# Optimization experiments

Hardware: AMD Instinct MI355X
Metric: run time of the kernel (lower is better)

The kernel has to match this reference:

```python
import jax, jax.numpy as jnp
import numpy as np

NHEADS = 8
HEAD_DIM = 64  # odim // nheads = 512 // 8


def setup_inputs() -> dict:
    key = jax.random.key(0)
    ks = jax.random.split(key, 5)
    B, S, D = 2, 4096, 512
    scale = 1.0 / np.sqrt(D)
    return {
        "m_feats": jax.random.normal(ks[0], (B, S, D), dtype=jnp.float32),
        "Wc": jax.random.normal(ks[1], (2 * D, D), dtype=jnp.float32) * scale,
        "bc": jax.random.normal(ks[2], (2 * D,), dtype=jnp.float32) * 0.01,
        "Wv": jax.random.normal(ks[3], (D, D), dtype=jnp.float32) * scale,
        "bv": jax.random.normal(ks[4], (D,), dtype=jnp.float32) * 0.01,
    }


def reference(m_feats, Wc, bc, Wv, bv):
    # eval mode: dropout(p=0.5) is identity
    B, S, D = m_feats.shape
    H, Dh = NHEADS, HEAD_DIM
    m_k = m_feats @ Wv.T + bv                    # [B,S,D]
    m_trans = m_feats @ Wc.T + bc                # [B,S,2D]
    m_q, m_v = m_trans[..., :D], m_trans[..., D:]
    # torch.split into contiguous per-head chunks == reshape to [B,S,H,Dh]
    k = m_k.reshape(B, S, H, Dh)
    q = m_q.reshape(B, S, H, Dh)
    v = m_v.reshape(B, S, H, Dh)
    # scores[b,h,i,j] = k_i . q_j / sqrt(Dh); softmax over j (the q axis)
    scores = jnp.einsum("bihd,bjhd->bhij", k, q) / np.sqrt(Dh).astype(np.float32)
    w = jax.nn.softmax(scores, axis=-1)          # [B,H,S,S]
    r = jnp.einsum("bhij,bjhd->bihd", w, v).reshape(B, S, D)
    return m_feats + r
```

## Files before the change

### kernel.cpp

```cpp
#include <hip/hip_runtime.h>

#define MTOT 8192

typedef __attribute__((ext_vector_type(8))) short bf16x8;
typedef __attribute__((ext_vector_type(4))) float f32x4;

#if __has_builtin(__builtin_amdgcn_exp2f)
#define EXP2F __builtin_amdgcn_exp2f
#else
#define EXP2F exp2f
#endif

#define SC 0.18033688011112042f
#define LDP 72
#define CTS 136

static __device__ __forceinline__ unsigned short tb(float f) {
  union { float f; unsigned int i; } x;
  x.f = f;
  return (unsigned short)(x.i >> 16);
}
static __device__ __forceinline__ unsigned int pkt(float a, float b) {
  union { float f; unsigned int i; } xa, xb;
  xa.f = a; xb.f = b;
  return (xa.i >> 16) | (xb.i & 0xFFFF0000u);
}
static __device__ __forceinline__ bf16x8 ld8f32_bf16(const float* __restrict__ p) {
  f32x4 lo = *(const f32x4*)p;
  f32x4 hi = *(const f32x4*)(p + 4);
  union { unsigned int u[4]; bf16x8 v; } r;
  r.u[0] = pkt(lo[0], lo[1]);
  r.u[1] = pkt(lo[2], lo[3]);
  r.u[2] = pkt(hi[0], hi[1]);
  r.u[3] = pkt(hi[2], hi[3]);
  return r.v;
}

__global__ __launch_bounds__(256) void gemm_qvk(
    const float* __restrict__ mf,
    const float* __restrict__ Wc,
    const float* __restrict__ bc,
    const float* __restrict__ Wv,
    const float* __restrict__ bv,
    unsigned short* __restrict__ ws,
    int nct)
{
  const int bid = blockIdx.x;
  const int tn = bid % nct, tm = bid / nct;
  const int w = threadIdx.x >> 6, lane = threadIdx.x & 63;
  const int n = lane & 15, q = lane >> 4;

  __shared__ alignas(16) unsigned short smem[2 * 128 * LDP];
  unsigned short* As = smem;
  unsigned short* Bs = smem + 128 * LDP;

  f32x4 acc[4][4] = {};
  const int rowA0 = tm * 128, colB0 = tn * 128;
  const int sr = threadIdx.x >> 4;
  const int sc = (threadIdx.x & 15) * 4;

  for (int kc = 0; kc < 512; kc += 64) {
    __syncthreads();
#pragma unroll
    for (int rr = 0; rr < 8; ++rr) {
      const int row = rr * 16 + sr;
      f32x4 av = *(const f32x4*)(mf + (size_t)(rowA0 + row) * 512 + kc + sc);
      uint2 ap; ap.x = pkt(av[0], av[1]); ap.y = pkt(av[2], av[3]);
      *(uint2*)(&As[row * LDP + sc]) = ap;
      const int c = colB0 + row;
      const float* bsrc = (c < 1024) ? (Wc + (size_t)c * 512)
                                     : (Wv + (size_t)(c - 1024) * 512);
      f32x4 bvx = *(const f32x4*)(bsrc + kc + sc);
      uint2 bp; bp.x = pkt(bvx[0], bvx[1]); bp.y = pkt(bvx[2], bvx[3]);
      *(uint2*)(&Bs[row * LDP + sc]) = bp;
    }
    __syncthreads();
#pragma unroll
    for (int ks = 0; ks < 2; ++ks) {
      bf16x8 a[4], b[4];
#pragma unroll
      for (int si = 0; si < 4; ++si)
        a[si] = *(const bf16x8*)(&As[((w >> 1) * 64 + si * 16 + n) * LDP + ks * 32 + q * 8]);
#pragma unroll
      for (int sj = 0; sj < 4; ++sj)
        b[sj] = *(const bf16x8*)(&Bs[((w & 1) * 64 + sj * 16 + n) * LDP + ks * 32 + q * 8]);
#pragma unroll
      for (int si = 0; si < 4; ++si)
#pragma unroll
        for (int sj = 0; sj < 4; ++sj)
          acc[si][sj] = __builtin_amdgcn_mfma_f32_16x16x32_bf16(a[si], b[sj], acc[si][sj], 0, 0, 0);
    }
  }

  __syncthreads();
  unsigned short* Ct = smem;
  const bool isV = (tn >= 4 && tn < 8);
  const int rl0 = (w >> 1) * 64, cl0 = (w & 1) * 64;

  if (!isV) {
    const bool isK = (tn >= 8);
#pragma unroll
    for (int sj = 0; sj < 4; ++sj) {
      const int c = colB0 + sj * 16 + n;
      const float bias = isK ? bv[c - 1024] : bc[c];
#pragma unroll
      for (int si = 0; si < 4; ++si)
#pragma unroll
        for (int r = 0; r < 4; ++r) {
          float v = acc[si][sj][r] + bias;
          if (isK) v *= SC;
          Ct[(rl0 + si * 16 + q * 4 + r) * CTS + cl0 + sj * 16 + n] = tb(v);
        }
    }
  } else {
#pragma unroll
    for (int sj = 0; sj < 4; ++sj) {
      const float bias = bc[colB0 + sj * 16 + n];
#pragma unroll
      for (int si = 0; si < 4; ++si) {
        uint2 pk;
        pk.x = pkt(acc[si][sj][0] + bias, acc[si][sj][1] + bias);
        pk.y = pkt(acc[si][sj][2] + bias, acc[si][sj][3] + bias);
        *(uint2*)(&Ct[(cl0 + sj * 16 + n) * CTS + rl0 + si * 16 + q * 4]) = pk;
      }
    }
  }
  __syncthreads();

  const int rk = threadIdx.x & 7, rr2 = threadIdx.x >> 3;
#pragma unroll
  for (int rp = 0; rp < 4; ++rp) {
    const int row = rp * 32 + rr2;
#pragma unroll
    for (int ch = 0; ch < 2; ++ch) {
      const int col = ch * 64 + rk * 8;
      bf16x8 v = *(const bf16x8*)(&Ct[row * CTS + col]);
      if (!isV) {
        const int srow = rowA0 + row;
        const int bb = srow >> 12, ss = srow & 4095;
        const int cg = colB0 + col;
        const int cl = (cg >= 1024) ? (cg - 1024) : cg;
        const int hh = cl >> 6, dh0 = cl & 63;
        unsigned short* base = (cg >= 1024) ? (ws + (size_t)2 * MTOT * 512) : ws;
        *(bf16x8*)(base + ((size_t)((bb * 8 + hh) * 4096 + ss)) * 64 + dh0) = v;
      } else {
        const int cv = (tn - 4) * 128 + row;
        const int hh = cv >> 6, dh0 = cv & 63;
        const int sg = rowA0 + col;
        const int bb = sg >> 12, ss = sg & 4095;
        *(bf16x8*)(ws + (size_t)MTOT * 512 +
                   ((size_t)((bb * 8 + hh) * 64 + dh0)) * 4096 + ss) = v;
      }
    }
  }
}

template <bool KWS>
__global__ __launch_bounds__(128, 2) void attn_kernel(
    const unsigned short* __restrict__ qvws,
    const float* __restrict__ mf,
    const float* __restrict__ Wv,
    const float* __restrict__ bv,
    float* __restrict__ out)
{
  const int bid = blockIdx.x;
  const int bh = ((bid & 7) << 1) | ((bid >> 3) & 1);
  const int ib = bid >> 4;
  const int b_ = bh >> 3, h = bh & 7;
  const int w = threadIdx.x >> 6, lane = threadIdx.x & 63;
  const int n = lane & 15, q = lane >> 4;
  const int i0 = ib * 64;

  __shared__ alignas(16) unsigned short PK[2][64 * LDP];
  __shared__ float lbuf[64];

  const unsigned short* Qb = qvws + (size_t)(bh * 4096) * 64;
  const unsigned short* Vb = qvws + (size_t)MTOT * 512 + (size_t)(bh * 64) * 4096;

  bf16x8 aK[4][2];
  if (KWS) {
    const unsigned short* Kb = qvws + (size_t)2 * MTOT * 512 + (size_t)(bh * 4096) * 64;
#pragma unroll
    for (int sub = 0; sub < 4; ++sub)
#pragma unroll
      for (int s = 0; s < 2; ++s)
        aK[sub][s] = *(const bf16x8*)(Kb + (size_t)(i0 + sub * 16 + n) * 64 + s * 32 + q * 8);
  } else {
    f32x4 ka[2][4] = {};
    for (int kk = 0; kk < 512; kk += 32) {
      bf16x8 a0 = ld8f32_bf16(mf + (size_t)(b_ * 4096 + i0 + (2 * w + 0) * 16 + n) * 512 + kk + q * 8);
      bf16x8 a1 = ld8f32_bf16(mf + (size_t)(b_ * 4096 + i0 + (2 * w + 1) * 16 + n) * 512 + kk + q * 8);
#pragma unroll
      for (int t = 0; t < 4; ++t) {
        bf16x8 bw = ld8f32_bf16(Wv + (size_t)(h * 64 + t * 16 + n) * 512 + kk + q * 8);
        ka[0][t] = __builtin_amdgcn_mfma_f32_16x16x32_bf16(a0, bw, ka[0][t], 0, 0, 0);
        ka[1][t] = __builtin_amdgcn_mfma_f32_16x16x32_bf16(a1, bw, ka[1][t], 0, 0, 0);
      }
    }
#pragma unroll
    for (int sl = 0; sl < 2; ++sl)
#pragma unroll
      for (int t = 0; t < 4; ++t) {
        const float bias = bv[h * 64 + t * 16 + n];
#pragma unroll
        for (int r = 0; r < 4; ++r)
          PK[0][((2 * w + sl) * 16 + q * 4 + r) * LDP + t * 16 + n] =
              tb((ka[sl][t][r] + bias) * SC);
      }
    __syncthreads();
#pragma unroll
    for (int sub = 0; sub < 4; ++sub)
#pragma unroll
      for (int s = 0; s < 2; ++s)
        aK[sub][s] = *(const bf16x8*)(&PK[0][(sub * 16 + n) * LDP + s * 32 + q * 8]);
    __syncthreads();
  }

  f32x4 o[4][4] = {};
  f32x4 lacc[4] = {};
  const bf16x8 ones = {(short)0x3F80, (short)0x3F80, (short)0x3F80, (short)0x3F80,
                       (short)0x3F80, (short)0x3F80, (short)0x3F80, (short)0x3F80};
  unsigned short* Pw = &PK[w][0];
  const int jbase = w * 2048;

  bf16x8 bq[4][2], bvv[4][2];
#pragma unroll
  for (int jt = 0; jt < 4; ++jt)
#pragma unroll
    for (int s = 0; s < 2; ++s)
      bq[jt][s] = *(const bf16x8*)(Qb + (size_t)(jbase + jt * 16 + n) * 64 + s * 32 + q * 8);
#pragma unroll
  for (int t = 0; t < 4; ++t)
#pragma unroll
    for (int s = 0; s < 2; ++s)
      bvv[t][s] = *(const bf16x8*)(Vb + (size_t)(t * 16 + n) * 4096 + jbase + s * 32 + q * 8);

  for (int it = 0; it < 32; ++it) {
    const int j1 = jbase + ((it + 1) & 31) * 64;

#pragma unroll
    for (int sub = 0; sub < 4; ++sub) {
      f32x4 c[4] = {};
#pragma unroll
      for (int jt = 0; jt < 4; ++jt)
#pragma unroll
        for (int s = 0; s < 2; ++s)
          c[jt] = __builtin_amdgcn_mfma_f32_16x16x32_bf16(bq[jt][s], aK[sub][s], c[jt], 0, 0, 0);
#pragma unroll
      for (int jt = 0; jt < 4; ++jt) {
        uint2 pk;
        pk.x = pkt(EXP2F(c[jt][0]), EXP2F(c[jt][1]));
        pk.y = pkt(EXP2F(c[jt][2]), EXP2F(c[jt][3]));
        *(uint2*)(Pw + (sub * 16 + n) * LDP + jt * 16 + q * 4) = pk;
      }
    }

#pragma unroll
    for (int jt = 0; jt < 4; ++jt)
#pragma unroll
      for (int s = 0; s < 2; ++s)
        bq[jt][s] = *(const bf16x8*)(Qb + (size_t)(j1 + jt * 16 + n) * 64 + s * 32 + q * 8);

    asm volatile("s_waitcnt lgkmcnt(0)" ::: "memory");

#pragma unroll
    for (int s = 0; s < 2; ++s) {
#pragma unroll
      for (int sub = 0; sub < 4; ++sub) {
        bf16x8 pa = *(const bf16x8*)(Pw + (sub * 16 + n) * LDP + s * 32 + q * 8);
        lacc[sub] = __builtin_amdgcn_mfma_f32_16x16x32_bf16(pa, ones, lacc[sub], 0, 0, 0);
#pragma unroll
        for (int t = 0; t < 4; ++t)
          o[sub][t] = __builtin_amdgcn_mfma_f32_16x16x32_bf16(pa, bvv[t][s], o[sub][t], 0, 0, 0);
      }
    }

#pragma unroll
    for (int t = 0; t < 4; ++t)
#pragma unroll
      for (int s = 0; s < 2; ++s)
        bvv[t][s] = *(const bf16x8*)(Vb + (size_t)(t * 16 + n) * 4096 + j1 + s * 32 + q * 8);
  }

  __syncthreads();
  float* mO = (float*)&PK[0][0];
  const int ebase = (w == 0) ? 0 : 32;
  const int rbase = (w == 0) ? 32 : 0;
  const int esub0 = (w == 0) ? 2 : 0;
  const int ksub0 = (w == 0) ? 0 : 2;
#pragma unroll
  for (int sl = 0; sl < 2; ++sl) {
    const int sub = esub0 + sl;
#pragma unroll
    for (int t = 0; t < 4; ++t)
#pragma unroll
      for (int r = 0; r < 4; ++r)
        mO[(ebase + sl * 16 + q * 4 + r) * 68 + t * 16 + n] = o[sub][t][r];
    if (n == 0)
#pragma unroll
      for (int r = 0; r < 4; ++r)
        lbuf[ebase + sl * 16 + q * 4 + r] = lacc[sub][r];
  }
  __syncthreads();
#pragma unroll
  for (int sl = 0; sl < 2; ++sl) {
    const int sub = ksub0 + sl;
    float li[4];
#pragma unroll
    for (int r = 0; r < 4; ++r)
      li[r] = 1.0f / (lacc[sub][r] + lbuf[rbase + sl * 16 + q * 4 + r]);
#pragma unroll
    for (int t = 0; t < 4; ++t) {
#pragma unroll
      for (int r = 0; r < 4; ++r) {
        const int i = i0 + sub * 16 + q * 4 + r;
        const int dh = t * 16 + n;
        const size_t idx = (size_t)(b_ * 4096 + i) * 512 + h * 64 + dh;
        out[idx] = (o[sub][t][r] + mO[(rbase + sl * 16 + q * 4 + r) * 68 + t * 16 + n]) * li[r]
                   + mf[idx];
      }
    }
  }
}

extern "C" void kernel_launch(void* const* d_in, const int* in_sizes, int n_in,
                              void* d_out, int out_size, void* d_ws, size_t ws_size,
                              hipStream_t stream) {
  const float* mf = (const float*)d_in[0];
  const float* Wc = (const float*)d_in[1];
  const float* bc = (const float*)d_in[2];
  const float* Wv = (const float*)d_in[3];
  const float* bv = (const float*)d_in[4];
  float* out = (float*)d_out;
  unsigned short* ws = (unsigned short*)d_ws;

  const bool kws = ws_size >= (size_t)3 * MTOT * 512 * 2;
  const int nct = kws ? 12 : 8;

  gemm_qvk<<<64 * nct, 256, 0, stream>>>(mf, Wc, bc, Wv, bv, ws, nct);
  if (kws)
    attn_kernel<true><<<1024, 128, 0, stream>>>(ws, mf, Wv, bv, out);
  else
    attn_kernel<false><<<1024, 128, 0, stream>>>(ws, mf, Wv, bv, out);
}
```

Measured before the change: 248.3 us.

## Keep softmax probabilities in registers, prefetch GEMM tiles, vectorize attention epilogue

The attention inner loop no longer writes exp'd scores to LDS and reads them back. It packs them directly into MFMA A-operand registers, reordering V loads into two 64-bit halves so the register layout matches the P fragment. Q loads are double-buffered through an unrolled two-step loop. The projection GEMM now prefetches the next K-chunk of fp32 inputs into registers while MFMAs run on the current chunk. The attention epilogue stages results in LDS so the output and residual traffic uses coalesced 16-byte accesses. The cost is higher register pressure from the extra buffers.

```diff
diff --git a/kernel.cpp b/kernel.cpp
--- a/kernel.cpp
+++ b/kernel.cpp
@@ -14,6 +14,7 @@
 #define SC 0.18033688011112042f
 #define LDP 72
 #define CTS 136
+#define MOS 68
 
 static __device__ __forceinline__ unsigned short tb(float f) {
   union { float f; unsigned int i; } x;
@@ -33,6 +34,11 @@
   r.u[1] = pkt(lo[2], lo[3]);
   r.u[2] = pkt(hi[0], hi[1]);
   r.u[3] = pkt(hi[2], hi[3]);
+  return r.v;
+}
+static __device__ __forceinline__ bf16x8 comb64(uint2 lo, uint2 hi) {
+  union { uint2 p[2]; bf16x8 v; } r;
+  r.p[0] = lo; r.p[1] = hi;
   return r.v;
 }
 
@@ -57,24 +63,42 @@
   f32x4 acc[4][4] = {};
   const int rowA0 = tm * 128, colB0 = tn * 128;
   const int sr = threadIdx.x >> 4;
-  const int sc = (threadIdx.x & 15) * 4;
+  const int sc4 = (threadIdx.x & 15) * 4;
+
+  f32x4 avr[8], bvr[8];
+#pragma unroll
+  for (int rr = 0; rr < 8; ++rr) {
+    const int row = rr * 16 + sr;
+    avr[rr] = *(const f32x4*)(mf + (size_t)(rowA0 + row) * 512 + sc4);
+    const int cB = colB0 + row;
+    const float* bsrc = (cB < 1024) ? (Wc + (size_t)cB * 512)
+                                    : (Wv + (size_t)(cB - 1024) * 512);
+    bvr[rr] = *(const f32x4*)(bsrc + sc4);
+  }
 
   for (int kc = 0; kc < 512; kc += 64) {
     __syncthreads();
 #pragma unroll
     for (int rr = 0; rr < 8; ++rr) {
       const int row = rr * 16 + sr;
-      f32x4 av = *(const f32x4*)(mf + (size_t)(rowA0 + row) * 512 + kc + sc);
-      uint2 ap; ap.x = pkt(av[0], av[1]); ap.y = pkt(av[2], av[3]);
-      *(uint2*)(&As[row * LDP + sc]) = ap;
-      const int c = colB0 + row;
-      const float* bsrc = (c < 1024) ? (Wc + (size_t)c * 512)
-                                     : (Wv + (size_t)(c - 1024) * 512);
-      f32x4 bvx = *(const f32x4*)(bsrc + kc + sc);
-      uint2 bp; bp.x = pkt(bvx[0], bvx[1]); bp.y = pkt(bvx[2], bvx[3]);
-      *(uint2*)(&Bs[row * LDP + sc]) = bp;
+      uint2 ap; ap.x = pkt(avr[rr][0], avr[rr][1]); ap.y = pkt(avr[rr][2], avr[rr][3]);
+      *(uint2*)(&As[row * LDP + sc4]) = ap;
+      uint2 bp; bp.x = pkt(bvr[rr][0], bvr[rr][1]); bp.y = pkt(bvr[rr][2], bvr[rr][3]);
+      *(uint2*)(&Bs[row * LDP + sc4]) = bp;
     }
     __syncthreads();
+    if (kc + 64 < 512) {
+      const int kn = kc + 64;
+#pragma unroll
+      for (int rr = 0; rr < 8; ++rr) {
+        const int row = rr * 16 + sr;
+        avr[rr] = *(const f32x4*)(mf + (size_t)(rowA0 + row) * 512 + kn + sc4);
+        const int cB = colB0 + row;
+        const float* bsrc = (cB < 1024) ? (Wc + (size_t)cB * 512)
+                                        : (Wv + (size_t)(cB - 1024) * 512);
+        bvr[rr] = *(const f32x4*)(bsrc + kn + sc4);
+      }
+    }
 #pragma unroll
     for (int ks = 0; ks < 2; ++ks) {
       bf16x8 a[4], b[4];
@@ -171,7 +195,7 @@
   const int n = lane & 15, q = lane >> 4;
   const int i0 = ib * 64;
 
-  __shared__ alignas(16) unsigned short PK[2][64 * LDP];
+  __shared__ alignas(16) float mO[64 * MOS];
   __shared__ float lbuf[64];
 
   const unsigned short* Qb = qvws + (size_t)(bh * 4096) * 64;
@@ -186,6 +210,7 @@
       for (int s = 0; s < 2; ++s)
         aK[sub][s] = *(const bf16x8*)(Kb + (size_t)(i0 + sub * 16 + n) * 64 + s * 32 + q * 8);
   } else {
+    unsigned short* Ks = (unsigned short*)mO;
     f32x4 ka[2][4] = {};
     for (int kk = 0; kk < 512; kk += 32) {
       bf16x8 a0 = ld8f32_bf16(mf + (size_t)(b_ * 4096 + i0 + (2 * w + 0) * 16 + n) * 512 + kk + q * 8);
@@ -204,7 +229,7 @@
         const float bias = bv[h * 64 + t * 16 + n];
 #pragma unroll
         for (int r = 0; r < 4; ++r)
-          PK[0][((2 * w + sl) * 16 + q * 4 + r) * LDP + t * 16 + n] =
+          Ks[((2 * w + sl) * 16 + q * 4 + r) * LDP + t * 16 + n] =
               tb((ka[sl][t][r] + bias) * SC);
       }
     __syncthreads();
@@ -212,7 +237,7 @@
     for (int sub = 0; sub < 4; ++sub)
 #pragma unroll
       for (int s = 0; s < 2; ++s)
-        aK[sub][s] = *(const bf16x8*)(&PK[0][(sub * 16 + n) * LDP + s * 32 + q * 8]);
+        aK[sub][s] = *(const bf16x8*)(&Ks[(sub * 16 + n) * LDP + s * 32 + q * 8]);
     __syncthreads();
   }
 
@@ -220,23 +245,28 @@
   f32x4 lacc[4] = {};
   const bf16x8 ones = {(short)0x3F80, (short)0x3F80, (short)0x3F80, (short)0x3F80,
                        (short)0x3F80, (short)0x3F80, (short)0x3F80, (short)0x3F80};
-  unsigned short* Pw = &PK[w][0];
   const int jbase = w * 2048;
 
-  bf16x8 bq[4][2], bvv[4][2];
+  bf16x8 bqA[4][2], bqB[4][2], bvv[4][2];
 #pragma unroll
   for (int jt = 0; jt < 4; ++jt)
 #pragma unroll
     for (int s = 0; s < 2; ++s)
-      bq[jt][s] = *(const bf16x8*)(Qb + (size_t)(jbase + jt * 16 + n) * 64 + s * 32 + q * 8);
+      bqA[jt][s] = *(const bf16x8*)(Qb + (size_t)(jbase + jt * 16 + n) * 64 + s * 32 + q * 8);
 #pragma unroll
   for (int t = 0; t < 4; ++t)
 #pragma unroll
-    for (int s = 0; s < 2; ++s)
-      bvv[t][s] = *(const bf16x8*)(Vb + (size_t)(t * 16 + n) * 4096 + jbase + s * 32 + q * 8);
-
-  for (int it = 0; it < 32; ++it) {
-    const int j1 = jbase + ((it + 1) & 31) * 64;
+    for (int s = 0; s < 2; ++s) {
+      const unsigned short* p0 = Vb + (size_t)(t * 16 + n) * 4096 + jbase + 32 * s + 4 * q;
+      bvv[t][s] = comb64(*(const uint2*)p0, *(const uint2*)(p0 + 16));
+    }
+
+  auto body = [&](bf16x8 (&bqc)[4][2], bf16x8 (&bqn)[4][2], int jn) {
+#pragma unroll
+    for (int jt = 0; jt < 4; ++jt)
+#pragma unroll
+      for (int s = 0; s < 2; ++s)
+        bqn[jt][s] = *(const bf16x8*)(Qb + (size_t)(jn + jt * 16 + n) * 64 + s * 32 + q * 8);
 
 #pragma unroll
     for (int sub = 0; sub < 4; ++sub) {
@@ -245,81 +275,80 @@
       for (int jt = 0; jt < 4; ++jt)
 #pragma unroll
         for (int s = 0; s < 2; ++s)
-          c[jt] = __builtin_amdgcn_mfma_f32_16x16x32_bf16(bq[jt][s], aK[sub][s], c[jt], 0, 0, 0);
-#pragma unroll
-      for (int jt = 0; jt < 4; ++jt) {
-        uint2 pk;
-        pk.x = pkt(EXP2F(c[jt][0]), EXP2F(c[jt][1]));
-        pk.y = pkt(EXP2F(c[jt][2]), EXP2F(c[jt][3]));
-        *(uint2*)(Pw + (sub * 16 + n) * LDP + jt * 16 + q * 4) = pk;
-      }
-    }
-
-#pragma unroll
-    for (int jt = 0; jt < 4; ++jt)
-#pragma unroll
-      for (int s = 0; s < 2; ++s)
-        bq[jt][s] = *(const bf16x8*)(Qb + (size_t)(j1 + jt * 16 + n) * 64 + s * 32 + q * 8);
-
-    asm volatile("s_waitcnt lgkmcnt(0)" ::: "memory");
-
-#pragma unroll
-    for (int s = 0; s < 2; ++s) {
-#pragma unroll
-      for (int sub = 0; sub < 4; ++sub) {
-        bf16x8 pa = *(const bf16x8*)(Pw + (sub * 16 + n) * LDP + s * 32 + q * 8);
-        lacc[sub] = __builtin_amdgcn_mfma_f32_16x16x32_bf16(pa, ones, lacc[sub], 0, 0, 0);
+          c[jt] = __builtin_amdgcn_mfma_f32_16x16x32_bf16(bqc[jt][s], aK[sub][s], c[jt], 0, 0, 0);
+      bf16x8 pa[2];
+#pragma unroll
+      for (int s = 0; s < 2; ++s) {
+        union { unsigned int u[4]; bf16x8 v; } p;
+        p.u[0] = pkt(EXP2F(c[2 * s][0]), EXP2F(c[2 * s][1]));
+        p.u[1] = pkt(EXP2F(c[2 * s][2]), EXP2F(c[2 * s][3]));
+        p.u[2] = pkt(EXP2F(c[2 * s + 1][0]), EXP2F(c[2 * s + 1][1]));
+        p.u[3] = pkt(EXP2F(c[2 * s + 1][2]), EXP2F(c[2 * s + 1][3]));
+        pa[s] = p.v;
+      }
+#pragma unroll
+      for (int s = 0; s < 2; ++s) {
+        lacc[sub] = __builtin_amdgcn_mfma_f32_16x16x32_bf16(pa[s], ones, lacc[sub], 0, 0, 0);
 #pragma unroll
         for (int t = 0; t < 4; ++t)
-          o[sub][t] = __builtin_amdgcn_mfma_f32_16x16x32_bf16(pa, bvv[t][s], o[sub][t], 0, 0, 0);
-      }
-    }
-
+          o[sub][t] = __builtin_amdgcn_mfma_f32_16x16x32_bf16(pa[s], bvv[t][s], o[sub][t], 0, 0, 0);
+      }
+    }
 #pragma unroll
     for (int t = 0; t < 4; ++t)
 #pragma unroll
-      for (int s = 0; s < 2; ++s)
-        bvv[t][s] = *(const bf16x8*)(Vb + (size_t)(t * 16 + n) * 4096 + j1 + s * 32 + q * 8);
-  }
-
-  __syncthreads();
-  float* mO = (float*)&PK[0][0];
-  const int ebase = (w == 0) ? 0 : 32;
-  const int rbase = (w == 0) ? 32 : 0;
-  const int esub0 = (w == 0) ? 2 : 0;
-  const int ksub0 = (w == 0) ? 0 : 2;
+      for (int s = 0; s < 2; ++s) {
+        const unsigned short* p0 = Vb + (size_t)(t * 16 + n) * 4096 + jn + 32 * s + 4 * q;
+        bvv[t][s] = comb64(*(const uint2*)p0, *(const uint2*)(p0 + 16));
+      }
+  };
+
+  for (int it = 0; it < 32; it += 2) {
+    body(bqA, bqB, jbase + ((it + 1) & 31) * 64);
+    body(bqB, bqA, jbase + ((it + 2) & 31) * 64);
+  }
+
+  __syncthreads();
+  const int eb = w ? 0 : 32, es0 = w ? 0 : 2;
+  const int kb = w ? 32 : 0, ks0 = w ? 2 : 0;
 #pragma unroll
   for (int sl = 0; sl < 2; ++sl) {
-    const int sub = esub0 + sl;
+    const int sub = es0 + sl;
 #pragma unroll
     for (int t = 0; t < 4; ++t)
 #pragma unroll
       for (int r = 0; r < 4; ++r)
-        mO[(ebase + sl * 16 + q * 4 + r) * 68 + t * 16 + n] = o[sub][t][r];
+        mO[(eb + sl * 16 + q * 4 + r) * MOS + t * 16 + n] = o[sub][t][r];
     if (n == 0)
 #pragma unroll
       for (int r = 0; r < 4; ++r)
-        lbuf[ebase + sl * 16 + q * 4 + r] = lacc[sub][r];
+        lbuf[eb + sl * 16 + q * 4 + r] = lacc[sub][r];
   }
   __syncthreads();
 #pragma unroll
   for (int sl = 0; sl < 2; ++sl) {
-    const int sub = ksub0 + sl;
+    const int sub = ks0 + sl;
     float li[4];
 #pragma unroll
     for (int r = 0; r < 4; ++r)
-      li[r] = 1.0f / (lacc[sub][r] + lbuf[rbase + sl * 16 + q * 4 + r]);
-#pragma unroll
-    for (int t = 0; t < 4; ++t) {
+      li[r] = 1.0f / (lacc[sub][r] + lbuf[kb + sl * 16 + q * 4 + r]);
+#pragma unroll
+    for (int t = 0; t < 4; ++t)
 #pragma unroll
       for (int r = 0; r < 4; ++r) {
-        const int i = i0 + sub * 16 + q * 4 + r;
-        const int dh = t * 16 + n;
-        const size_t idx = (size_t)(b_ * 4096 + i) * 512 + h * 64 + dh;
-        out[idx] = (o[sub][t][r] + mO[(rbase + sl * 16 + q * 4 + r) * 68 + t * 16 + n]) * li[r]
-                   + mf[idx];
-      }
-    }
+        const int mrow = kb + sl * 16 + q * 4 + r;
+        const int mcol = t * 16 + n;
+        mO[mrow * MOS + mcol] = (o[sub][t][r] + mO[mrow * MOS + mcol]) * li[r];
+      }
+  }
+  __syncthreads();
+  const int orow = threadIdx.x >> 1, ohalf = (threadIdx.x & 1) * 32;
+  const size_t obase = (size_t)(b_ * 4096 + i0 + orow) * 512 + h * 64 + ohalf;
+#pragma unroll
+  for (int c4 = 0; c4 < 8; ++c4) {
+    f32x4 v = *(const f32x4*)(&mO[orow * MOS + ohalf + c4 * 4]);
+    f32x4 m = *(const f32x4*)(mf + obase + c4 * 4);
+    *(f32x4*)(out + obase + c4 * 4) = v + m;
   }
 }
 
```

New measurement: 293.0 us. 1.18x slower.
